# Performance work log

Hardware: AMD Instinct MI355X
Metric: run time of the kernel (lower is better)

The kernel has to match this reference:

```python
import math
import jax, jax.numpy as jnp
import numpy as np

B, L, D = 8, 512, 512          # batch, seq, d_model
G, S = 8, 4                    # n_groups, expert_scale (clones per group)
FG, FE = 4, 64                 # features per group, d_feat_emb
E = G * S                      # n_experts = 32
DH, RH = 256, 256              # d_expert_hidden, d_router_hidden
TEMP, SHARP, BIAS = 1.0, 16.0, 1.0
GK, SK = 2, 2                  # group_top_k, expert_top_k


def setup_inputs() -> dict:
    key = jax.random.key(0)
    ks = jax.random.split(key, 12)
    def n(k, shape, fan_in):
        return (jax.random.normal(k, shape) * (fan_in ** -0.5)).astype(jnp.float32)
    return {
        "hidden": jax.random.normal(ks[0], (B, L, D), jnp.float32),
        "feat": jax.random.uniform(ks[1], (B, L, G * FG), dtype=jnp.float32),
        "valid_mask": jnp.ones((B, L), jnp.bool_),
        # outer (group) router: hidden -> RH -> G
        "Wr1": n(ks[2], (D, RH), D), "br1": jnp.zeros((RH,), jnp.float32),
        "Wr2": n(ks[3], (RH, G), RH), "br2": jnp.zeros((G,), jnp.float32),
        # per-group feature embedding: FG -> FE
        "Wfe": n(ks[4], (G, FG, FE), FG), "bfe": jnp.zeros((G, FE), jnp.float32),
        # per-group inner (clone) router on [hidden ; feat_emb] -> S
        "Win_h": n(ks[5], (G, D, S), D + FE),
        "Win_f": n(ks[6], (G, FE, S), D + FE),
        "bin_b": jnp.zeros((G, S), jnp.float32),
        # per-expert MLP: D -> DH -> D
        "We1": n(ks[7], (E, D, DH), D), "be1": jnp.zeros((E, DH), jnp.float32),
        "We2": n(ks[8], (E, DH, D), DH), "be2": jnp.zeros((E, D), jnp.float32),
    }


def _to_ratio(x):
    # faithful to _to_ratio: clamp if already in [0,1], else Gaussian CDF
    clamped = jnp.clip(x, 0.0, 1.0)
    cdf = jnp.clip(0.5 * (1.0 + jax.lax.erf(x / math.sqrt(2.0))), 0.0, 1.0)
    in01 = jnp.logical_and(x.min() >= -1e-6, x.max() <= 1.0 + 1e-6)
    return jnp.where(in01, clamped, cdf)


def _topk_softmax(logits, k):
    # softmax over top-k entries, zeros elsewhere (== scatter of softmax(top_vals))
    vals, _ = jax.lax.top_k(logits, k)
    thresh = vals[..., -1:]
    neg = jnp.finfo(logits.dtype).min
    return jax.nn.softmax(jnp.where(logits >= thresh, logits, neg), axis=-1)


def _forward(hidden, feat, Wr1, br1, Wr2, br2, Wfe, bfe, Win_h, Win_f, bin_b,
             We1, be1, We2, be2):
    gelu = lambda x: jax.nn.gelu(x, approximate=False)  # torch nn.GELU default
    # ---- outer (group) router: hidden-only, token mode ----
    gh = gelu(hidden @ Wr1 + br1)                       # [B,L,RH]
    glog = (gh @ Wr2 + br2) / TEMP                      # [B,L,G]
    gw = _topk_softmax(glog, GK)                        # [B,L,G]
    # ---- inner rule teacher: bins over normalized group feature ratios ----
    feat_g = feat.reshape(B, L, G, FG)
    score = _to_ratio(feat_g).mean(-1, keepdims=True)   # [B,L,G,1]
    centers = jnp.linspace(0.0, 1.0, S, dtype=jnp.float32)
    rule = -SHARP * (score - centers) ** 2              # [B,L,G,S]
    # ---- inner (clone) router: hidden + group feature embedding + rule bias ----
    femb = jnp.einsum('blgf,gfe->blge', feat_g, Wfe) + bfe          # [B,L,G,FE]
    ilog = (jnp.einsum('bld,gds->blgs', hidden, Win_h)
            + jnp.einsum('blge,ges->blgs', femb, Win_f)
            + bin_b + BIAS * rule) / TEMP                            # [B,L,G,S]
    cw = _topk_softmax(ilog, SK)                                     # [B,L,G,S]
    # ---- combine hierarchical weights (group-major expert order) ----
    w = (gw[..., None] * cw).reshape(B, L, E)                        # [B,L,E]
    # ---- dense grouped expert MLPs (dropout=0 at eval) ----
    h1 = gelu(jnp.einsum('bld,edh->bleh', hidden, We1) + be1)        # [B,L,E,DH]
    y = jnp.einsum('bleh,ehd,ble->bld', h1, We2, w)
    y = y + jnp.einsum('ble,ed->bld', w, be2)
    return y


def reference(hidden, feat, valid_mask, Wr1, br1, Wr2, br2, Wfe, bfe,
              Win_h, Win_f, bin_b, We1, be1, We2, be2):
    del valid_mask  # token-mode routing; mask only used for session pooling
    return _forward(hidden, feat, Wr1, br1, Wr2, br2, Wfe, bfe,
                    Win_h, Win_f, bin_b, We1, be1, We2, be2)
```

## Files before the change

### kernel.cpp

```cpp
#include <hip/hip_runtime.h>
#include <hip/hip_bf16.h>
#include <math.h>

#define BB   8
#define LL   512
#define DD   512
#define GG   8
#define SSS  4
#define FGC  4
#define FEC  64
#define EEC  32
#define DHC  256
#define RHC  256
#define NT   (BB*LL)
#define TM   32
#define TR   8

#define XC_STRIDE 264
#define CPAD 32

typedef __attribute__((ext_vector_type(8))) short short8;
typedef __attribute__((ext_vector_type(4))) float floatx4;

__device__ __forceinline__ float gelu_exact(float x) {
    return 0.5f * x * (1.0f + erff(x * 0.70710678118654752440f));
}

__device__ __forceinline__ unsigned pk2(float a, float b) {
    union { __hip_bfloat162 h; unsigned u; } cv;
    cv.h = __float22bfloat162_rn(make_float2(a, b));
    return cv.u;
}
union U4S8 { unsigned u[4]; short8 s; };

__device__ __forceinline__ floatx4 mfma16(short8 a, short8 b, floatx4 c) {
    return __builtin_amdgcn_mfma_f32_16x16x32_bf16(a, b, c, 0, 0, 0);
}

__global__ __launch_bounds__(256) void prep_kernel(
    const float* __restrict__ Win_h, const float* __restrict__ Win_f,
    const float* __restrict__ Wfe, const float* __restrict__ bfe,
    const float* __restrict__ bin_b,
    float* __restrict__ WinT, float* __restrict__ M2, float* __restrict__ c2b)
{
    const int tid = threadIdx.x;
    if (blockIdx.x < 64) {
        int idx = blockIdx.x * 256 + tid;
        int d = idx >> 5, gs = idx & 31;
        int g = gs >> 2, s = gs & 3;
        WinT[idx] = Win_h[(size_t)g*DD*SSS + d*SSS + s];
    } else {
        if (tid < GG*FGC*SSS) {
            int g = tid >> 4, f = (tid >> 2) & 3, s = tid & 3;
            float acc = 0.f;
            for (int e = 0; e < FEC; ++e)
                acc += Wfe[(size_t)g*FGC*FEC + f*FEC + e] * Win_f[(size_t)g*FEC*SSS + e*SSS + s];
            M2[tid] = acc;
        } else if (tid < GG*FGC*SSS + GG*SSS) {
            int gs = tid - GG*FGC*SSS;
            int g = gs >> 2, s = gs & 3;
            float acc = bin_b[gs];
            for (int e = 0; e < FEC; ++e)
                acc += bfe[g*FEC + e] * Win_f[(size_t)g*FEC*SSS + e*SSS + s];
            c2b[gs] = acc;
        }
    }
}

__global__ __launch_bounds__(256) void pack_weights(
    const float* __restrict__ We1, const float* __restrict__ We2,
    short* __restrict__ Wp1, short* __restrict__ Wp2)
{
    const int gid = blockIdx.x * 256 + threadIdx.x;
    if (gid < EEC*16*16*64) {
        const int lane = gid & 63;
        const int nb   = (gid >> 6) & 15;
        const int i    = (gid >> 10) & 15;
        const int e    = gid >> 14;
        const int k0   = i*32 + (lane >> 4)*8;
        const int n    = nb*16 + (lane & 15);
        const float* s = We1 + ((size_t)e*DD + k0)*DHC + n;
        float f[8];
        #pragma unroll
        for (int j = 0; j < 8; ++j) f[j] = s[(size_t)j*DHC];
        U4S8 cv;
        cv.u[0] = pk2(f[0], f[1]); cv.u[1] = pk2(f[2], f[3]);
        cv.u[2] = pk2(f[4], f[5]); cv.u[3] = pk2(f[6], f[7]);
        *(short8*)(Wp1 + (size_t)gid*8) = cv.s;
    } else {
        const int g2   = gid - EEC*16*16*64;
        const int lane = g2 & 63;
        const int nb   = (g2 >> 6) & 31;
        const int i    = (g2 >> 11) & 7;
        const int e    = g2 >> 14;
        const int k0   = i*32 + (lane >> 4)*8;
        const int n    = nb*16 + (lane & 15);
        const float* s = We2 + ((size_t)e*DHC + k0)*DD + n;
        float f[8];
        #pragma unroll
        for (int j = 0; j < 8; ++j) f[j] = s[(size_t)j*DD];
        U4S8 cv;
        cv.u[0] = pk2(f[0], f[1]); cv.u[1] = pk2(f[2], f[3]);
        cv.u[2] = pk2(f[4], f[5]); cv.u[3] = pk2(f[6], f[7]);
        *(short8*)(Wp2 + (size_t)g2*8) = cv.s;
    }
}

__global__ __launch_bounds__(256) void fused_route(
    const float* __restrict__ hidden, const float* __restrict__ feat,
    const float* __restrict__ Wr1, const float* __restrict__ br1,
    const float* __restrict__ Wr2, const float* __restrict__ br2,
    const float* __restrict__ WinT, const float* __restrict__ M2,
    const float* __restrict__ c2b,
    int* __restrict__ bucket_tok, float* __restrict__ bucket_w,
    int* __restrict__ counts, int* __restrict__ nslot)
{
    const int t0  = blockIdx.x * TR;
    const int tid = threadIdx.x;

    __shared__ float hs[TR][DD];
    __shared__ float ghs[TR][RHC+4];
    __shared__ float featb[TR][GG*FGC];
    __shared__ float glogp[TR][GG][4];
    __shared__ float gwvb[TR][GG];
    __shared__ float scoreb[TR][GG];
    __shared__ float ilogb[TR][GG*SSS];
    __shared__ float cwvb[TR][GG*SSS];

    for (int i = tid; i < TR*DD; i += 256) {
        int r = i >> 9, c = i & 511;
        hs[r][c] = hidden[(size_t)(t0 + r)*DD + c];
    }
    if (tid < TR*GG*FGC) {
        int r = tid >> 5, c = tid & 31;
        featb[r][c] = feat[(t0 + r)*(GG*FGC) + c];
    }
    __syncthreads();

    if (tid < TR*GG) {
        int t = tid >> 3, g = tid & 7;
        float s = 0.f;
        #pragma unroll
        for (int f = 0; f < FGC; ++f) s += fminf(fmaxf(featb[t][g*4+f], 0.f), 1.f);
        scoreb[t][g] = s * 0.25f;
    }

    {
        float acc[TR];
        float b = br1[tid];
        #pragma unroll
        for (int t = 0; t < TR; ++t) acc[t] = b;
        #pragma unroll 4
        for (int k = 0; k < DD; k += 4) {
            float w0 = Wr1[(size_t)k*RHC + tid];
            float w1 = Wr1[(size_t)(k+1)*RHC + tid];
            float w2 = Wr1[(size_t)(k+2)*RHC + tid];
            float w3 = Wr1[(size_t)(k+3)*RHC + tid];
            #pragma unroll
            for (int t = 0; t < TR; ++t) {
                float4 h = *(const float4*)(&hs[t][k]);
                acc[t] += h.x*w0 + h.y*w1 + h.z*w2 + h.w*w3;
            }
        }
        #pragma unroll
        for (int t = 0; t < TR; ++t) ghs[t][tid] = gelu_exact(acc[t]);
    }
    __syncthreads();

    {
        const int t = tid >> 5, g = (tid >> 2) & 7, q = tid & 3;
        float s = (q == 0) ? br2[g] : 0.f;
        const float* wr = Wr2 + g;
        #pragma unroll 4
        for (int h = q*64; h < q*64 + 64; ++h) s += ghs[t][h] * wr[(size_t)h*GG];
        glogp[t][g][q] = s;
    }

    {
        const int t = tid >> 5, gs = tid & 31;
        const int g = gs >> 2, s = gs & 3;
        float acc = 0.f;
        #pragma unroll 8
        for (int k = 0; k < DD; ++k) acc += hs[t][k] * WinT[k*32 + gs];
        const float* m2 = M2 + g*16 + s;
        acc += featb[t][g*4+0]*m2[0] + featb[t][g*4+1]*m2[4]
             + featb[t][g*4+2]*m2[8] + featb[t][g*4+3]*m2[12];
        const float centers[4] = {0.0f, 1.0f/3.0f, 2.0f/3.0f, 1.0f};
        float diff = scoreb[t][g] - centers[s];
        ilogb[t][gs] = acc + c2b[gs] - 16.0f * diff * diff;
    }
    __syncthreads();

    if (tid < TR) {
        int t = tid;
        float gl[GG];
        #pragma unroll
        for (int g = 0; g < GG; ++g)
            gl[g] = glogp[t][g][0] + glogp[t][g][1] + glogp[t][g][2] + glogp[t][g][3];
        float a = -INFINITY, b = -INFINITY;
        #pragma unroll
        for (int g = 0; g < GG; ++g) {
            float v = gl[g];
            if (v > a) { b = a; a = v; } else if (v > b) { b = v; }
        }
        float thresh = b, m = a, sum = 0.f;
        float ex[GG];
        #pragma unroll
        for (int g = 0; g < GG; ++g) {
            ex[g] = (gl[g] >= thresh) ? __expf(gl[g] - m) : 0.f;
            sum += ex[g];
        }
        float inv = 1.0f / sum;
        #pragma unroll
        for (int g = 0; g < GG; ++g) gwvb[t][g] = ex[g] * inv;
    }
    if (tid < TR*GG) {
        int t = tid >> 3, g = tid & 7;
        float vv[4] = {ilogb[t][g*4+0], ilogb[t][g*4+1], ilogb[t][g*4+2], ilogb[t][g*4+3]};
        float a = -INFINITY, b = -INFINITY;
        #pragma unroll
        for (int s = 0; s < 4; ++s) {
            float v = vv[s];
            if (v > a) { b = a; a = v; } else if (v > b) { b = v; }
        }
        float thresh = b, m = a, sum = 0.f;
        float ex[4];
        #pragma unroll
        for (int s = 0; s < 4; ++s) {
            ex[s] = (vv[s] >= thresh) ? __expf(vv[s] - m) : 0.f;
            sum += ex[s];
        }
        float inv = 1.0f / sum;
        #pragma unroll
        for (int s = 0; s < 4; ++s) cwvb[t][g*4 + s] = ex[s] * inv;
    }
    __syncthreads();

    if (tid < TR) {
        int t = tid;
        int a = 0;
        for (int g = 0; g < GG; ++g) {
            float gw = gwvb[t][g];
            if (gw > 0.f) {
                for (int s = 0; s < SSS; ++s) {
                    float w = gw * cwvb[t][g*4 + s];
                    if (w > 0.f && a < 4) {
                        int ee = g*SSS + s;
                        int pos = atomicAdd(&counts[ee*CPAD], 1);
                        bucket_tok[ee*NT + pos] = ((t0 + t) << 2) | a;
                        bucket_w[ee*NT + pos]   = w;
                        ++a;
                    }
                }
            }
        }
        nslot[t0 + t] = a;
    }
}

__global__ __launch_bounds__(256) void expert_mfma4(
    const float* __restrict__ hidden,
    const short* __restrict__ Wp1, const float* __restrict__ be1,
    const short* __restrict__ Wp2, const float* __restrict__ be2,
    const int* __restrict__ bucket_tok, const float* __restrict__ bucket_w,
    const int* __restrict__ counts,
    float* __restrict__ y_part)
{
    const int e    = blockIdx.x & 31;
    const int tile = blockIdx.x >> 5;
    const int cnt  = counts[e*CPAD];
    const int r0   = tile * TM;
    if (r0 >= cnt) return;
    const int nrow = min(TM, cnt - r0);
    const int tid  = threadIdx.x;
    const int wave = tid >> 6;
    const int lane = tid & 63;
    const int lm   = lane & 15;
    const int quad = lane >> 4;

    __shared__ short Xp[64 * XC_STRIDE];
    __shared__ short Hp[32 * XC_STRIDE];
    __shared__ int   toks[TM];
    __shared__ float tws[TM];

    if (tid < TM) {
        if (tid < nrow) {
            toks[tid] = bucket_tok[e*NT + r0 + tid];
            tws[tid]  = bucket_w[e*NT + r0 + tid];
        } else { toks[tid] = -1; tws[tid] = 0.f; }
    }
    __syncthreads();

    {
        const int xr = tid >> 3;
        const int xk = tid & 7;
        const int bt = toks[xr];
        const float* src = hidden + (size_t)(bt < 0 ? 0 : (bt >> 2))*DD;
        #pragma unroll
        for (int i = 0; i < 8; ++i) {
            const int k8 = xk + 8*i;
            float4 v0 = make_float4(0.f,0.f,0.f,0.f), v1 = v0;
            if (bt >= 0) {
                v0 = *(const float4*)(src + k8*8);
                v1 = *(const float4*)(src + k8*8 + 4);
            }
            U4S8 cv;
            cv.u[0] = pk2(v0.x, v0.y); cv.u[1] = pk2(v0.z, v0.w);
            cv.u[2] = pk2(v1.x, v1.y); cv.u[3] = pk2(v1.z, v1.w);
            *(short8*)(&Xp[k8 * XC_STRIDE + xr * 8]) = cv.s;
        }
    }
    __syncthreads();

    floatx4 acc[2][4];
    #pragma unroll
    for (int mb = 0; mb < 2; ++mb)
        #pragma unroll
        for (int nb = 0; nb < 4; ++nb)
            acc[mb][nb] = (floatx4){0.f, 0.f, 0.f, 0.f};

    const short* W1 = Wp1 + (size_t)e * (16*16*64*8);

    for (int i = 0; i < 16; ++i) {
        const int k8 = i*4 + quad;
        short8 a0 = *(const short8*)(&Xp[k8 * XC_STRIDE + lm * 8]);
        short8 a1 = *(const short8*)(&Xp[k8 * XC_STRIDE + (16 + lm) * 8]);
        const short* wb = W1 + ((size_t)i*16 + wave*4)*512 + lane*8;
        #pragma unroll
        for (int nb = 0; nb < 4; ++nb) {
            short8 b = *(const short8*)(wb + nb*512);
            acc[0][nb] = mfma16(a0, b, acc[0][nb]);
            acc[1][nb] = mfma16(a1, b, acc[1][nb]);
        }
    }

    #pragma unroll
    for (int nb = 0; nb < 4; ++nb) {
        const int h = wave*64 + nb*16 + lm;
        const float b1 = be1[e*DHC + h];
        #pragma unroll
        for (int mb = 0; mb < 2; ++mb) {
            #pragma unroll
            for (int r = 0; r < 4; r += 2) {
                const int m0 = mb*16 + quad*4 + r;
                unsigned u = pk2(gelu_exact(acc[mb][nb][r]   + b1),
                                 gelu_exact(acc[mb][nb][r+1] + b1));
                Hp[(h >> 3) * XC_STRIDE + m0 * 8 + (h & 7)]     = (short)(u & 0xffff);
                Hp[(h >> 3) * XC_STRIDE + (m0+1) * 8 + (h & 7)] = (short)(u >> 16);
            }
        }
    }
    __syncthreads();

    floatx4 c[2][8];
    #pragma unroll
    for (int mb = 0; mb < 2; ++mb)
        #pragma unroll
        for (int nb = 0; nb < 8; ++nb)
            c[mb][nb] = (floatx4){0.f, 0.f, 0.f, 0.f};

    const short* W2 = Wp2 + (size_t)e * (8*32*64*8);

    for (int i = 0; i < 8; ++i) {
        const int k8 = i*4 + quad;
        short8 a0 = *(const short8*)(&Hp[k8 * XC_STRIDE + lm * 8]);
        short8 a1 = *(const short8*)(&Hp[k8 * XC_STRIDE + (16 + lm) * 8]);
        const short* wb = W2 + ((size_t)i*32 + wave*8)*512 + lane*8;
        #pragma unroll
        for (int nb = 0; nb < 8; ++nb) {
            short8 b = *(const short8*)(wb + nb*512);
            c[0][nb] = mfma16(a0, b, c[0][nb]);
            c[1][nb] = mfma16(a1, b, c[1][nb]);
        }
    }

    #pragma unroll
    for (int nb = 0; nb < 8; ++nb) {
        const int col = wave*128 + nb*16 + lm;
        const float b2 = be2[e*DD + col];
        #pragma unroll
        for (int mb = 0; mb < 2; ++mb) {
            #pragma unroll
            for (int r = 0; r < 4; ++r) {
                const int m = mb*16 + quad*4 + r;
                const int bt = toks[m];
                if (bt >= 0)
                    y_part[(size_t)bt*DD + col] = tws[m] * (c[mb][nb][r] + b2);
            }
        }
    }
}

__global__ __launch_bounds__(256) void reduce_y(
    const float* __restrict__ y_part, const int* __restrict__ nslot,
    float* __restrict__ y)
{
    const int idx = blockIdx.x * 256 + threadIdx.x;
    const int t  = idx >> 7;
    const int c4 = idx & 127;
    const int ns = nslot[t];
    float4 s = make_float4(0.f, 0.f, 0.f, 0.f);
    const float* p = y_part + ((size_t)t*4)*DD + c4*4;
    for (int a = 0; a < ns; ++a) {
        float4 v = *(const float4*)(p + (size_t)a*DD);
        s.x += v.x; s.y += v.y; s.z += v.z; s.w += v.w;
    }
    *(float4*)(y + (size_t)t*DD + c4*4) = s;
}

__global__ __launch_bounds__(256) void expert_mfma3(
    const float* __restrict__ hidden,
    const float* __restrict__ We1, const float* __restrict__ be1,
    const float* __restrict__ We2, const float* __restrict__ be2,
    const int* __restrict__ bucket_tok, const float* __restrict__ bucket_w,
    const int* __restrict__ counts,
    float* __restrict__ y)
{
    const int e    = blockIdx.x & 31;
    const int tile = blockIdx.x >> 5;
    const int cnt  = counts[e*CPAD];
    const int r0   = tile * TM;
    if (r0 >= cnt) return;
    const int nrow = min(TM, cnt - r0);
    const int tid  = threadIdx.x;
    const int wave = tid >> 6;
    const int lane = tid & 63;
    const int lm   = lane & 15;
    const int quad = lane >> 4;

    __shared__ short Xp[64 * XC_STRIDE];
    __shared__ short Hp[32 * XC_STRIDE];
    __shared__ int   toks[TM];
    __shared__ float tws[TM];

    if (tid < TM) {
        if (tid < nrow) {
            toks[tid] = bucket_tok[e*NT + r0 + tid] >> 2;
            tws[tid]  = bucket_w[e*NT + r0 + tid];
        } else { toks[tid] = -1; tws[tid] = 0.f; }
    }
    __syncthreads();

    {
        const int xr = tid >> 3;
        const int xk = tid & 7;
        const int tk = toks[xr];
        const float* src = hidden + (size_t)(tk < 0 ? 0 : tk)*DD;
        #pragma unroll
        for (int i = 0; i < 8; ++i) {
            const int k8 = xk + 8*i;
            float4 v0 = make_float4(0.f,0.f,0.f,0.f), v1 = v0;
            if (tk >= 0) {
                v0 = *(const float4*)(src + k8*8);
                v1 = *(const float4*)(src + k8*8 + 4);
            }
            U4S8 cv;
            cv.u[0] = pk2(v0.x, v0.y); cv.u[1] = pk2(v0.z, v0.w);
            cv.u[2] = pk2(v1.x, v1.y); cv.u[3] = pk2(v1.z, v1.w);
            *(short8*)(&Xp[k8 * XC_STRIDE + xr * 8]) = cv.s;
        }
    }
    __syncthreads();

    floatx4 acc[2][4];
    #pragma unroll
    for (int mb = 0; mb < 2; ++mb)
        #pragma unroll
        for (int nb = 0; nb < 4; ++nb)
            acc[mb][nb] = (floatx4){0.f, 0.f, 0.f, 0.f};

    const float* W1 = We1 + (size_t)e * DD * DHC;

    for (int i = 0; i < 16; ++i) {
        const int k8 = i*4 + quad;
        short8 a0 = *(const short8*)(&Xp[k8 * XC_STRIDE + lm * 8]);
        short8 a1 = *(const short8*)(&Xp[k8 * XC_STRIDE + (16 + lm) * 8]);
        float wreg[4][8];
        #pragma unroll
        for (int nb = 0; nb < 4; ++nb) {
            const float* s = W1 + (size_t)(k8*8)*DHC + wave*64 + nb*16 + lm;
            #pragma unroll
            for (int j = 0; j < 8; ++j) wreg[nb][j] = s[(size_t)j*DHC];
        }
        #pragma unroll
        for (int nb = 0; nb < 4; ++nb) {
            U4S8 cv;
            cv.u[0] = pk2(wreg[nb][0], wreg[nb][1]);
            cv.u[1] = pk2(wreg[nb][2], wreg[nb][3]);
            cv.u[2] = pk2(wreg[nb][4], wreg[nb][5]);
            cv.u[3] = pk2(wreg[nb][6], wreg[nb][7]);
            acc[0][nb] = mfma16(a0, cv.s, acc[0][nb]);
            acc[1][nb] = mfma16(a1, cv.s, acc[1][nb]);
        }
    }

    #pragma unroll
    for (int nb = 0; nb < 4; ++nb) {
        const int h = wave*64 + nb*16 + lm;
        const float b1 = be1[e*DHC + h];
        #pragma unroll
        for (int mb = 0; mb < 2; ++mb) {
            #pragma unroll
            for (int r = 0; r < 4; r += 2) {
                const int m0 = mb*16 + quad*4 + r;
                unsigned u = pk2(gelu_exact(acc[mb][nb][r]   + b1),
                                 gelu_exact(acc[mb][nb][r+1] + b1));
                Hp[(h >> 3) * XC_STRIDE + m0 * 8 + (h & 7)]     = (short)(u & 0xffff);
                Hp[(h >> 3) * XC_STRIDE + (m0+1) * 8 + (h & 7)] = (short)(u >> 16);
            }
        }
    }
    __syncthreads();

    floatx4 c[2][8];
    #pragma unroll
    for (int mb = 0; mb < 2; ++mb)
        #pragma unroll
        for (int nb = 0; nb < 8; ++nb)
            c[mb][nb] = (floatx4){0.f, 0.f, 0.f, 0.f};

    const float* W2 = We2 + (size_t)e * DHC * DD;

    for (int i = 0; i < 8; ++i) {
        const int k8 = i*4 + quad;
        short8 a0 = *(const short8*)(&Hp[k8 * XC_STRIDE + lm * 8]);
        short8 a1 = *(const short8*)(&Hp[k8 * XC_STRIDE + (16 + lm) * 8]);
        #pragma unroll
        for (int half = 0; half < 2; ++half) {
            float wreg[4][8];
            #pragma unroll
            for (int nb4 = 0; nb4 < 4; ++nb4) {
                const int n = wave*128 + (half*4 + nb4)*16 + lm;
                const float* s = W2 + (size_t)(k8*8)*DD + n;
                #pragma unroll
                for (int j = 0; j < 8; ++j) wreg[nb4][j] = s[(size_t)j*DD];
            }
            #pragma unroll
            for (int nb4 = 0; nb4 < 4; ++nb4) {
                const int nb = half*4 + nb4;
                U4S8 cv;
                cv.u[0] = pk2(wreg[nb4][0], wreg[nb4][1]);
                cv.u[1] = pk2(wreg[nb4][2], wreg[nb4][3]);
                cv.u[2] = pk2(wreg[nb4][4], wreg[nb4][5]);
                cv.u[3] = pk2(wreg[nb4][6], wreg[nb4][7]);
                c[0][nb] = mfma16(a0, cv.s, c[0][nb]);
                c[1][nb] = mfma16(a1, cv.s, c[1][nb]);
            }
        }
    }

    #pragma unroll
    for (int nb = 0; nb < 8; ++nb) {
        const int col = wave*128 + nb*16 + lm;
        const float b2 = be2[e*DD + col];
        #pragma unroll
        for (int mb = 0; mb < 2; ++mb) {
            #pragma unroll
            for (int r = 0; r < 4; ++r) {
                const int m = mb*16 + quad*4 + r;
                const int tk = toks[m];
                if (tk >= 0)
                    atomicAdd(&y[(size_t)tk*DD + col], tws[m] * (c[mb][nb][r] + b2));
            }
        }
    }
}

extern "C" void kernel_launch(void* const* d_in, const int* in_sizes, int n_in,
                              void* d_out, int out_size, void* d_ws, size_t ws_size,
                              hipStream_t stream) {
    const float* hidden = (const float*)d_in[0];
    const float* feat   = (const float*)d_in[1];
    const float* Wr1    = (const float*)d_in[3];
    const float* br1    = (const float*)d_in[4];
    const float* Wr2    = (const float*)d_in[5];
    const float* br2    = (const float*)d_in[6];
    const float* Wfe    = (const float*)d_in[7];
    const float* bfe    = (const float*)d_in[8];
    const float* Win_h  = (const float*)d_in[9];
    const float* Win_f  = (const float*)d_in[10];
    const float* bin_b  = (const float*)d_in[11];
    const float* We1    = (const float*)d_in[12];
    const float* be1    = (const float*)d_in[13];
    const float* We2    = (const float*)d_in[14];
    const float* be2    = (const float*)d_in[15];
    float* y = (float*)d_out;

    char* ws = (char*)d_ws;
    int*   bucket_tok = (int*)ws;    ws += (size_t)EEC*NT*sizeof(int);
    float* bucket_w   = (float*)ws;  ws += (size_t)EEC*NT*sizeof(float);
    int*   counts     = (int*)ws;    ws += (size_t)EEC*CPAD*sizeof(int);
    float* WinT       = (float*)ws;  ws += (size_t)DD*EEC*sizeof(float);
    float* M2         = (float*)ws;  ws += 512;
    float* c2b        = (float*)ws;  ws += 256;
    int*   nslot      = (int*)ws;    ws += (size_t)NT*sizeof(int);
    size_t base_used  = (size_t)(ws - (char*)d_ws);

    short* Wp1    = (short*)ws;
    short* Wp2    = Wp1 + (size_t)EEC*DD*DHC;
    float* y_part = (float*)(Wp2 + (size_t)EEC*DHC*DD);
    size_t need_fast = base_used
                     + 2*(size_t)EEC*DD*DHC*sizeof(short)
                     + (size_t)NT*4*DD*sizeof(float);
    const bool fast = (ws_size >= need_fast);

    hipMemsetAsync(counts, 0, EEC*CPAD*sizeof(int), stream);

    prep_kernel<<<65, 256, 0, stream>>>(Win_h, Win_f, Wfe, bfe, bin_b,
                                        WinT, M2, c2b);

    if (fast) {
        pack_weights<<<4096, 256, 0, stream>>>(We1, We2, Wp1, Wp2);

        fused_route<<<NT/TR, 256, 0, stream>>>(hidden, feat, Wr1, br1, Wr2, br2,
                                               WinT, M2, c2b,
                                               bucket_tok, bucket_w, counts, nslot);

        expert_mfma4<<<(NT/TM)*EEC, 256, 0, stream>>>(hidden, Wp1, be1, Wp2, be2,
                                                      bucket_tok, bucket_w, counts,
                                                      y_part);

        reduce_y<<<(NT*DD/4)/256, 256, 0, stream>>>(y_part, nslot, y);
    } else {
        hipMemsetAsync(y, 0, (size_t)NT*DD*sizeof(float), stream);

        fused_route<<<NT/TR, 256, 0, stream>>>(hidden, feat, Wr1, br1, Wr2, br2,
                                               WinT, M2, c2b,
                                               bucket_tok, bucket_w, counts, nslot);

        expert_mfma3<<<(NT/TM)*EEC, 256, 0, stream>>>(hidden, We1, be1, We2, be2,
                                                      bucket_tok, bucket_w, counts, y);
    }
}
```

Before: 295.3 us.

## Use compact expert tile worklist with persistent grid and prefetch weight fragments

Adds a tiny kernel that turns per-expert token counts into a compact list of (expert, tile) work items. The expert kernel now runs a fixed persistent grid that loops over this list, so it no longer launches 4096 blocks of which most exit early. It also double-buffers the B-operand weight fragments in registers so the global loads for the next k-step overlap the current MFMAs. This costs one extra launch and more register use, and the block-to-item mapping changes how weights are reused across the cache.

```diff
diff --git a/kernel.cpp b/kernel.cpp
--- a/kernel.cpp
+++ b/kernel.cpp
@@ -18,6 +18,8 @@
 
 #define XC_STRIDE 264
 #define CPAD 32
+#define NWL_MAX 4096
+#define EGRID 1024
 
 typedef __attribute__((ext_vector_type(8))) short short8;
 typedef __attribute__((ext_vector_type(4))) float floatx4;
@@ -258,20 +260,36 @@
     }
 }
 
-__global__ __launch_bounds__(256) void expert_mfma4(
+__global__ __launch_bounds__(64) void build_worklist(
+    const int* __restrict__ counts, int* __restrict__ worklist,
+    int* __restrict__ nwork)
+{
+    __shared__ int tiles[EEC], offs[EEC];
+    const int tid = threadIdx.x;
+    if (tid < EEC) tiles[tid] = (counts[tid*CPAD] + TM - 1) / TM;
+    __syncthreads();
+    if (tid == 0) {
+        int acc = 0;
+        for (int e = 0; e < EEC; ++e) { offs[e] = acc; acc += tiles[e]; }
+        nwork[0] = acc;
+    }
+    __syncthreads();
+    if (tid < EEC) {
+        const int n = tiles[tid], o = offs[tid];
+        for (int t = 0; t < n; ++t) worklist[o + t] = (tid << 16) | t;
+    }
+}
+
+__global__ __launch_bounds__(256) void expert_mfma5(
     const float* __restrict__ hidden,
     const short* __restrict__ Wp1, const float* __restrict__ be1,
     const short* __restrict__ Wp2, const float* __restrict__ be2,
     const int* __restrict__ bucket_tok, const float* __restrict__ bucket_w,
     const int* __restrict__ counts,
+    const int* __restrict__ worklist, const int* __restrict__ nwork,
     float* __restrict__ y_part)
 {
-    const int e    = blockIdx.x & 31;
-    const int tile = blockIdx.x >> 5;
-    const int cnt  = counts[e*CPAD];
-    const int r0   = tile * TM;
-    if (r0 >= cnt) return;
-    const int nrow = min(TM, cnt - r0);
+    const int NW   = nwork[0];
     const int tid  = threadIdx.x;
     const int wave = tid >> 6;
     const int lane = tid & 63;
@@ -283,111 +301,150 @@
     __shared__ int   toks[TM];
     __shared__ float tws[TM];
 
-    if (tid < TM) {
-        if (tid < nrow) {
-            toks[tid] = bucket_tok[e*NT + r0 + tid];
-            tws[tid]  = bucket_w[e*NT + r0 + tid];
-        } else { toks[tid] = -1; tws[tid] = 0.f; }
-    }
-    __syncthreads();
-
-    {
-        const int xr = tid >> 3;
-        const int xk = tid & 7;
-        const int bt = toks[xr];
-        const float* src = hidden + (size_t)(bt < 0 ? 0 : (bt >> 2))*DD;
-        #pragma unroll
+    for (int it = blockIdx.x; it < NW; it += EGRID) {
+        const int item = worklist[it];
+        const int e    = item >> 16;
+        const int tile = item & 0xffff;
+        const int cnt  = counts[e*CPAD];
+        const int r0   = tile * TM;
+        const int nrow = min(TM, cnt - r0);
+
+        const short* W1 = Wp1 + (size_t)e * (16*16*64*8);
+        const short* W2 = Wp2 + (size_t)e * (8*32*64*8);
+
+        if (tid < TM) {
+            if (tid < nrow) {
+                toks[tid] = bucket_tok[e*NT + r0 + tid];
+                tws[tid]  = bucket_w[e*NT + r0 + tid];
+            } else { toks[tid] = -1; tws[tid] = 0.f; }
+        }
+
+        short8 b1c[4];
+        {
+            const short* wb = W1 + ((size_t)wave*4)*512 + lane*8;
+            #pragma unroll
+            for (int nb = 0; nb < 4; ++nb) b1c[nb] = *(const short8*)(wb + nb*512);
+        }
+        __syncthreads();
+
+        {
+            const int xr = tid >> 3;
+            const int xk = tid & 7;
+            const int bt = toks[xr];
+            const float* src = hidden + (size_t)(bt < 0 ? 0 : (bt >> 2))*DD;
+            #pragma unroll
+            for (int i = 0; i < 8; ++i) {
+                const int k8 = xk + 8*i;
+                float4 v0 = make_float4(0.f,0.f,0.f,0.f), v1 = v0;
+                if (bt >= 0) {
+                    v0 = *(const float4*)(src + k8*8);
+                    v1 = *(const float4*)(src + k8*8 + 4);
+                }
+                U4S8 cv;
+                cv.u[0] = pk2(v0.x, v0.y); cv.u[1] = pk2(v0.z, v0.w);
+                cv.u[2] = pk2(v1.x, v1.y); cv.u[3] = pk2(v1.z, v1.w);
+                *(short8*)(&Xp[k8 * XC_STRIDE + xr * 8]) = cv.s;
+            }
+        }
+        __syncthreads();
+
+        floatx4 acc[2][4];
+        #pragma unroll
+        for (int mb = 0; mb < 2; ++mb)
+            #pragma unroll
+            for (int nb = 0; nb < 4; ++nb)
+                acc[mb][nb] = (floatx4){0.f, 0.f, 0.f, 0.f};
+
+        for (int i = 0; i < 16; ++i) {
+            const int k8 = i*4 + quad;
+            short8 b1n[4];
+            if (i < 15) {
+                const short* wb = W1 + ((size_t)(i+1)*16 + wave*4)*512 + lane*8;
+                #pragma unroll
+                for (int nb = 0; nb < 4; ++nb) b1n[nb] = *(const short8*)(wb + nb*512);
+            }
+            short8 a0 = *(const short8*)(&Xp[k8 * XC_STRIDE + lm * 8]);
+            short8 a1 = *(const short8*)(&Xp[k8 * XC_STRIDE + (16 + lm) * 8]);
+            #pragma unroll
+            for (int nb = 0; nb < 4; ++nb) {
+                acc[0][nb] = mfma16(a0, b1c[nb], acc[0][nb]);
+                acc[1][nb] = mfma16(a1, b1c[nb], acc[1][nb]);
+            }
+            if (i < 15) {
+                #pragma unroll
+                for (int nb = 0; nb < 4; ++nb) b1c[nb] = b1n[nb];
+            }
+        }
+
+        short8 b2c[8];
+        {
+            const short* wb = W2 + ((size_t)wave*8)*512 + lane*8;
+            #pragma unroll
+            for (int nb = 0; nb < 8; ++nb) b2c[nb] = *(const short8*)(wb + nb*512);
+        }
+
+        #pragma unroll
+        for (int nb = 0; nb < 4; ++nb) {
+            const int h = wave*64 + nb*16 + lm;
+            const float b1 = be1[e*DHC + h];
+            #pragma unroll
+            for (int mb = 0; mb < 2; ++mb) {
+                #pragma unroll
+                for (int r = 0; r < 4; r += 2) {
+                    const int m0 = mb*16 + quad*4 + r;
+                    unsigned u = pk2(gelu_exact(acc[mb][nb][r]   + b1),
+                                     gelu_exact(acc[mb][nb][r+1] + b1));
+                    Hp[(h >> 3) * XC_STRIDE + m0 * 8 + (h & 7)]     = (short)(u & 0xffff);
+                    Hp[(h >> 3) * XC_STRIDE + (m0+1) * 8 + (h & 7)] = (short)(u >> 16);
+                }
+            }
+        }
+        __syncthreads();
+
+        floatx4 c[2][8];
+        #pragma unroll
+        for (int mb = 0; mb < 2; ++mb)
+            #pragma unroll
+            for (int nb = 0; nb < 8; ++nb)
+                c[mb][nb] = (floatx4){0.f, 0.f, 0.f, 0.f};
+
         for (int i = 0; i < 8; ++i) {
-            const int k8 = xk + 8*i;
-            float4 v0 = make_float4(0.f,0.f,0.f,0.f), v1 = v0;
-            if (bt >= 0) {
-                v0 = *(const float4*)(src + k8*8);
-                v1 = *(const float4*)(src + k8*8 + 4);
-            }
-            U4S8 cv;
-            cv.u[0] = pk2(v0.x, v0.y); cv.u[1] = pk2(v0.z, v0.w);
-            cv.u[2] = pk2(v1.x, v1.y); cv.u[3] = pk2(v1.z, v1.w);
-            *(short8*)(&Xp[k8 * XC_STRIDE + xr * 8]) = cv.s;
-        }
-    }
-    __syncthreads();
-
-    floatx4 acc[2][4];
-    #pragma unroll
-    for (int mb = 0; mb < 2; ++mb)
-        #pragma unroll
-        for (int nb = 0; nb < 4; ++nb)
-            acc[mb][nb] = (floatx4){0.f, 0.f, 0.f, 0.f};
-
-    const short* W1 = Wp1 + (size_t)e * (16*16*64*8);
-
-    for (int i = 0; i < 16; ++i) {
-        const int k8 = i*4 + quad;
-        short8 a0 = *(const short8*)(&Xp[k8 * XC_STRIDE + lm * 8]);
-        short8 a1 = *(const short8*)(&Xp[k8 * XC_STRIDE + (16 + lm) * 8]);
-        const short* wb = W1 + ((size_t)i*16 + wave*4)*512 + lane*8;
-        #pragma unroll
-        for (int nb = 0; nb < 4; ++nb) {
-            short8 b = *(const short8*)(wb + nb*512);
-            acc[0][nb] = mfma16(a0, b, acc[0][nb]);
-            acc[1][nb] = mfma16(a1, b, acc[1][nb]);
-        }
-    }
-
-    #pragma unroll
-    for (int nb = 0; nb < 4; ++nb) {
-        const int h = wave*64 + nb*16 + lm;
-        const float b1 = be1[e*DHC + h];
-        #pragma unroll
-        for (int mb = 0; mb < 2; ++mb) {
-            #pragma unroll
-            for (int r = 0; r < 4; r += 2) {
-                const int m0 = mb*16 + quad*4 + r;
-                unsigned u = pk2(gelu_exact(acc[mb][nb][r]   + b1),
-                                 gelu_exact(acc[mb][nb][r+1] + b1));
-                Hp[(h >> 3) * XC_STRIDE + m0 * 8 + (h & 7)]     = (short)(u & 0xffff);
-                Hp[(h >> 3) * XC_STRIDE + (m0+1) * 8 + (h & 7)] = (short)(u >> 16);
-            }
-        }
-    }
-    __syncthreads();
-
-    floatx4 c[2][8];
-    #pragma unroll
-    for (int mb = 0; mb < 2; ++mb)
-        #pragma unroll
-        for (int nb = 0; nb < 8; ++nb)
-            c[mb][nb] = (floatx4){0.f, 0.f, 0.f, 0.f};
-
-    const short* W2 = Wp2 + (size_t)e * (8*32*64*8);
-
-    for (int i = 0; i < 8; ++i) {
-        const int k8 = i*4 + quad;
-        short8 a0 = *(const short8*)(&Hp[k8 * XC_STRIDE + lm * 8]);
-        short8 a1 = *(const short8*)(&Hp[k8 * XC_STRIDE + (16 + lm) * 8]);
-        const short* wb = W2 + ((size_t)i*32 + wave*8)*512 + lane*8;
+            const int k8 = i*4 + quad;
+            short8 b2n[8];
+            if (i < 7) {
+                const short* wb = W2 + ((size_t)(i+1)*32 + wave*8)*512 + lane*8;
+                #pragma unroll
+                for (int nb = 0; nb < 8; ++nb) b2n[nb] = *(const short8*)(wb + nb*512);
+            }
+            short8 a0 = *(const short8*)(&Hp[k8 * XC_STRIDE + lm * 8]);
+            short8 a1 = *(const short8*)(&Hp[k8 * XC_STRIDE + (16 + lm) * 8]);
+            #pragma unroll
+            for (int nb = 0; nb < 8; ++nb) {
+                c[0][nb] = mfma16(a0, b2c[nb], c[0][nb]);
+                c[1][nb] = mfma16(a1, b2c[nb], c[1][nb]);
+            }
+            if (i < 7) {
+                #pragma unroll
+                for (int nb = 0; nb < 8; ++nb) b2c[nb] = b2n[nb];
+            }
+        }
+
         #pragma unroll
         for (int nb = 0; nb < 8; ++nb) {
-            short8 b = *(const short8*)(wb + nb*512);
-            c[0][nb] = mfma16(a0, b, c[0][nb]);
-            c[1][nb] = mfma16(a1, b, c[1][nb]);
-        }
-    }
-
-    #pragma unroll
-    for (int nb = 0; nb < 8; ++nb) {
-        const int col = wave*128 + nb*16 + lm;
-        const float b2 = be2[e*DD + col];
-        #pragma unroll
-        for (int mb = 0; mb < 2; ++mb) {
-            #pragma unroll
-            for (int r = 0; r < 4; ++r) {
-                const int m = mb*16 + quad*4 + r;
-                const int bt = toks[m];
-                if (bt >= 0)
-                    y_part[(size_t)bt*DD + col] = tws[m] * (c[mb][nb][r] + b2);
-            }
-        }
+            const int col = wave*128 + nb*16 + lm;
+            const float b2 = be2[e*DD + col];
+            #pragma unroll
+            for (int mb = 0; mb < 2; ++mb) {
+                #pragma unroll
+                for (int r = 0; r < 4; ++r) {
+                    const int m = mb*16 + quad*4 + r;
+                    const int bt = toks[m];
+                    if (bt >= 0)
+                        y_part[(size_t)bt*DD + col] = tws[m] * (c[mb][nb][r] + b2);
+                }
+            }
+        }
+        __syncthreads();
     }
 }
 
@@ -594,6 +651,8 @@
     float* M2         = (float*)ws;  ws += 512;
     float* c2b        = (float*)ws;  ws += 256;
     int*   nslot      = (int*)ws;    ws += (size_t)NT*sizeof(int);
+    int*   worklist   = (int*)ws;    ws += (size_t)NWL_MAX*sizeof(int);
+    int*   nwork      = (int*)ws;    ws += 128;
     size_t base_used  = (size_t)(ws - (char*)d_ws);
 
     short* Wp1    = (short*)ws;
@@ -616,9 +675,11 @@
                                                WinT, M2, c2b,
                                                bucket_tok, bucket_w, counts, nslot);
 
-        expert_mfma4<<<(NT/TM)*EEC, 256, 0, stream>>>(hidden, Wp1, be1, Wp2, be2,
-                                                      bucket_tok, bucket_w, counts,
-                                                      y_part);
+        build_worklist<<<1, 64, 0, stream>>>(counts, worklist, nwork);
+
+        expert_mfma5<<<EGRID, 256, 0, stream>>>(hidden, Wp1, be1, Wp2, be2,
+                                                bucket_tok, bucket_w, counts,
+                                                worklist, nwork, y_part);
 
         reduce_y<<<(NT*DD/4)/256, 256, 0, stream>>>(y_part, nslot, y);
     } else {
```

Measured after the change: 262.7 us. -11.0%, faster.
